# Optimization experiments

Measured on AMD Instinct MI355X. Metric: run time of the kernel, lower is better.

The kernel has to match this reference:

```python
import jax, jax.numpy as jnp
import numpy as np

N = 1024
C = 50000
D = 128
M_MARGIN = 0.35
S_SCALE = 30.0
LAMDA = 0.01


def setup_inputs() -> dict:
    key = jax.random.key(0)
    k1, k2, k3 = jax.random.split(key, 3)
    feature = jax.random.normal(k1, (N, D), dtype=jnp.float32)
    weight = jax.random.normal(k2, (C, D), dtype=jnp.float32)
    label = jax.random.randint(k3, (N,), 0, C, dtype=jnp.int64)
    return {"feature": feature, "weight": weight, "label": label}


def reference(feature, weight, label):
    eps = 1e-8  # torch CosineSimilarity eps
    f = feature / jnp.maximum(jnp.linalg.norm(feature, axis=-1, keepdims=True), eps)
    w = weight / jnp.maximum(jnp.linalg.norm(weight, axis=-1, keepdims=True), eps)
    cos = jnp.einsum("nd,cd->nc", f, w)  # [N, C] cosine similarities
    onehot = jax.nn.one_hot(label, C, dtype=cos.dtype)  # [N, C]
    # CosFace: subtract margin m from the target-class cosine, scale by s
    logits = S_SCALE * (cos - M_MARGIN * onehot)
    target_logit = S_SCALE * (jnp.take_along_axis(cos, label[:, None], axis=1)[:, 0] - M_MARGIN)
    # -log( exp(t) / (exp(t) + sum_{j != y} exp(s*cos_j)) ) = logsumexp(logits) - t
    lse = jax.nn.logsumexp(logits, axis=-1)  # [N]
    loss_lmc = jnp.mean(lse - target_logit)
    # center loss: 0.5 * sum_i ||f_i - w_{y_i}||^2
    diff = feature - weight[label]
    loss_c = 0.5 * jnp.sum(diff * diff)
    return loss_lmc + LAMDA * loss_c
```

## Files before the change

kernel.cpp:

```cpp
#include <hip/hip_runtime.h>

#define N_ROWS   1024
#define D_DIM    128
#define C_CLS    50000
#define C_PAD    50048
#define NCT64    782
#define NG       128
#define NPART    256
#define S_SCALE  30.0f
#define M_MARGIN 0.35f
#define EXP2_SCALE 43.2808512266689f
#define EXP2M      15.1482979293341f
#define LN2        0.6931471805599453f

typedef short s8v __attribute__((ext_vector_type(8)));
typedef float f4v __attribute__((ext_vector_type(4)));

__device__ inline unsigned short f2bf(float f) {
    unsigned u = __float_as_uint(f);
    u += 0x7FFF + ((u >> 16) & 1);
    return (unsigned short)(u >> 16);
}
__device__ inline float bf2f(unsigned short h) {
    return __uint_as_float(((unsigned)h) << 16);
}
__device__ inline void load_lds16(const char* src, unsigned char* lds) {
    __builtin_amdgcn_global_load_lds(
        (const __attribute__((address_space(1))) void*)src,
        (__attribute__((address_space(3))) void*)lds, 16, 0, 0);
}

__global__ void norm_rows_fused(const float* __restrict__ weight,
                                const float* __restrict__ feature,
                                unsigned short* __restrict__ what,
                                unsigned short* __restrict__ fhat) {
    int wid = threadIdx.x >> 6, lane = threadIdx.x & 63;
    int half = lane >> 5, l32 = lane & 31;
    int B = blockIdx.x;

    const float* src;
    unsigned short* dst;
    int rowBase, isW;
    float scale;
    if (B < 6272) {
        int x = B & 7, q = B >> 3;
        int ct = x + 8 * (q >> 3);
        if (ct >= NCT64) return;
        rowBase = ct * 64 + (q & 7) * 8;
        src = weight; dst = what; scale = 1.0f; isW = 1;
    } else {
        rowBase = (B - 6272) * 8;
        src = feature; dst = fhat; scale = EXP2_SCALE; isW = 0;
    }

    int srcRow = rowBase + wid * 2 + half;
    int valid = isW ? (srcRow < C_CLS) : 1;

    float4 v = make_float4(0.f, 0.f, 0.f, 0.f);
    if (valid) v = ((const float4*)src)[(size_t)srcRow * 32 + l32];
    float ss = v.x * v.x + v.y * v.y + v.z * v.z + v.w * v.w;
    #pragma unroll
    for (int s = 1; s < 32; s <<= 1) ss += __shfl_xor(ss, s, 32);
    float inv = valid ? scale / fmaxf(sqrtf(ss), 1e-8f) : 0.f;
    ushort4 o;
    o.x = f2bf(v.x * inv); o.y = f2bf(v.y * inv);
    o.z = f2bf(v.z * inv); o.w = f2bf(v.w * inv);
    ((ushort4*)dst)[(size_t)srcRow * 32 + l32] = o;
}

__global__ __launch_bounds__(256, 3)
void gemm_exp_kernel(const short* __restrict__ fhat,
                     const short* __restrict__ what,
                     float* __restrict__ part2) {
    __shared__ __align__(16) unsigned char smem[32768];
    const int g   = blockIdx.x;
    const int rt  = blockIdx.y;
    const int tid = threadIdx.x;
    const int wid = tid >> 6;
    const int lane = tid & 63;
    const int lrow = lane & 15;
    const int kgrp = lane >> 4;
    const int wrow = wid >> 1;
    const int wcol = wid & 1;
    const int nt = (g < 14) ? 7 : 6;
    const int rot = ((g >> 3) + rt) % nt;

    const char* aSrc  = (const char*)fhat + (size_t)rt * 32768;
    const char* bBase = (const char*)what;

    #pragma unroll
    for (int i = 0; i < 8; i++) {
        int o = wid * 8192 + i * 1024 + lane * 16;
        int s = o ^ (((o >> 8) & 7) << 4);
        load_lds16(aSrc + s, smem + o);
    }
    __syncthreads();

    s8v afr[4][4];
    #pragma unroll
    for (int kk = 0; kk < 4; kk++)
        #pragma unroll
        for (int m = 0; m < 4; m++) {
            int row = wrow * 64 + m * 16 + lrow;
            int b = (row * 256 + kk * 64 + kgrp * 16) ^ ((row & 7) << 4);
            afr[kk][m] = *(const s8v*)(smem + b);
        }
    __syncthreads();

    int vb[2][4];
    #pragma unroll
    for (int n = 0; n < 2; n++)
        #pragma unroll
        for (int kk = 0; kk < 4; kk++) {
            int row = wcol * 32 + n * 16 + lrow;
            vb[n][kk] = (row * 256 + kk * 64 + kgrp * 16) ^ ((row & 7) << 4);
        }

    {
        const char* src = bBase + (size_t)(g + 128 * rot) * 16384;
        #pragma unroll
        for (int i = 0; i < 4; i++) {
            int o = wid * 4096 + i * 1024 + lane * 16;
            int s = o ^ (((o >> 8) & 7) << 4);
            load_lds16(src + s, smem + o);
        }
    }

    float esum[4][4];
    #pragma unroll
    for (int m = 0; m < 4; m++)
        #pragma unroll
        for (int j = 0; j < 4; j++) esum[m][j] = 0.f;

    const f4v FZERO = {0.f, 0.f, 0.f, 0.f};

    for (int i = 0; i < nt; ++i) {
        int t = i + rot; if (t >= nt) t -= nt;
        const int ct = g + 128 * t;
        __syncthreads();

        if (i + 1 < nt) {
            int tn = t + 1; if (tn >= nt) tn -= nt;
            const char* src = bBase + (size_t)(g + 128 * tn) * 16384;
            unsigned char* dstb = smem + ((i + 1) & 1) * 16384;
            #pragma unroll
            for (int ii = 0; ii < 4; ii++) {
                int o = wid * 4096 + ii * 1024 + lane * 16;
                int s = o ^ (((o >> 8) & 7) << 4);
                load_lds16(src + s, dstb + o);
            }
        }

        const unsigned char* bb = smem + (i & 1) * 16384;
        f4v acc[4][2];

        {
            s8v b0 = *(const s8v*)(bb + vb[0][0]);
            s8v b1 = *(const s8v*)(bb + vb[1][0]);
            #pragma unroll
            for (int m = 0; m < 4; m++) {
                acc[m][0] = __builtin_amdgcn_mfma_f32_16x16x32_bf16(
                    afr[0][m], b0, FZERO, 0, 0, 0);
                acc[m][1] = __builtin_amdgcn_mfma_f32_16x16x32_bf16(
                    afr[0][m], b1, FZERO, 0, 0, 0);
            }
        }
        #pragma unroll
        for (int kk = 1; kk < 4; kk++) {
            s8v b0 = *(const s8v*)(bb + vb[0][kk]);
            s8v b1 = *(const s8v*)(bb + vb[1][kk]);
            #pragma unroll
            for (int m = 0; m < 4; m++) {
                acc[m][0] = __builtin_amdgcn_mfma_f32_16x16x32_bf16(
                    afr[kk][m], b0, acc[m][0], 0, 0, 0);
                acc[m][1] = __builtin_amdgcn_mfma_f32_16x16x32_bf16(
                    afr[kk][m], b1, acc[m][1], 0, 0, 0);
            }
        }

        if (ct != NCT64 - 1) {
            #pragma unroll
            for (int m = 0; m < 4; m++)
                #pragma unroll
                for (int n = 0; n < 2; n++)
                    #pragma unroll
                    for (int j = 0; j < 4; j++)
                        esum[m][j] += __builtin_amdgcn_exp2f(acc[m][n][j]);
        } else {
            #pragma unroll
            for (int n = 0; n < 2; n++) {
                int gc = ct * 64 + wcol * 32 + n * 16 + lrow;
                #pragma unroll
                for (int m = 0; m < 4; m++)
                    #pragma unroll
                    for (int j = 0; j < 4; j++)
                        if (gc < C_CLS)
                            esum[m][j] += __builtin_amdgcn_exp2f(acc[m][n][j]);
            }
        }
    }

    #pragma unroll
    for (int m = 0; m < 4; m++)
        #pragma unroll
        for (int j = 0; j < 4; j++) {
            float v = esum[m][j];
            v += __shfl_xor(v, 1, 64);
            v += __shfl_xor(v, 2, 64);
            v += __shfl_xor(v, 4, 64);
            v += __shfl_xor(v, 8, 64);
            if (lrow == 0) {
                int row = rt * 128 + wrow * 64 + m * 16 + kgrp * 4 + j;
                part2[(size_t)row * NPART + g * 2 + wcol] = v;
            }
        }
}

__global__ void finalize_rows_kernel(const float* __restrict__ part2,
                                     const unsigned short* __restrict__ fhat,
                                     const unsigned short* __restrict__ what,
                                     const float* __restrict__ feature,
                                     const float* __restrict__ weight,
                                     const int* __restrict__ label,
                                     float* __restrict__ rowval) {
    int wid = threadIdx.x >> 6, lane = threadIdx.x & 63;
    int n = blockIdx.x * 4 + wid;
    int y = label[n];

    const float* p = part2 + (size_t)n * NPART;
    float S = p[lane] + p[64 + lane] + p[128 + lane] + p[192 + lane];

    float2 f2 = ((const float2*)feature)[(size_t)n * 64 + lane];
    float2 w2 = ((const float2*)weight)[(size_t)y * 64 + lane];
    float dx = f2.x - w2.x, dy = f2.y - w2.y;
    float cl = dx * dx + dy * dy;

    ushort2 fh = ((const ushort2*)fhat)[(size_t)n * 64 + lane];
    ushort2 wh = ((const ushort2*)what)[(size_t)y * 64 + lane];
    float cys = bf2f(fh.x) * bf2f(wh.x) + bf2f(fh.y) * bf2f(wh.y);

    #pragma unroll
    for (int s = 1; s < 64; s <<= 1) {
        S   += __shfl_xor(S, s, 64);
        cl  += __shfl_xor(cl, s, 64);
        cys += __shfl_xor(cys, s, 64);
    }
    if (lane == 0) {
        float t2 = cys - EXP2M;
        float Sp = S - __builtin_amdgcn_exp2f(cys) + __builtin_amdgcn_exp2f(t2);
        rowval[n] = (logf(Sp) - LN2 * t2) * (1.0f / (float)N_ROWS) + 0.005f * cl;
    }
}

__global__ void reduce_final_kernel(const float* __restrict__ rowval, float* __restrict__ out) {
    __shared__ float sbuf[4];
    int t = threadIdx.x;
    float v = rowval[t] + rowval[t + 256] + rowval[t + 512] + rowval[t + 768];
    #pragma unroll
    for (int s = 1; s < 64; s <<= 1) v += __shfl_xor(v, s, 64);
    if ((t & 63) == 0) sbuf[t >> 6] = v;
    __syncthreads();
    if (t == 0) out[0] = sbuf[0] + sbuf[1] + sbuf[2] + sbuf[3];
}

extern "C" void kernel_launch(void* const* d_in, const int* in_sizes, int n_in,
                              void* d_out, int out_size, void* d_ws, size_t ws_size,
                              hipStream_t stream) {
    const float* feature = (const float*)d_in[0];
    const float* weight  = (const float*)d_in[1];
    const int*   label   = (const int*)d_in[2];

    const size_t WS_NEEDED = 14127104;
    if (ws_size < WS_NEEDED) return;

    char* ws = (char*)d_ws;
    unsigned short* what = (unsigned short*)ws;
    unsigned short* fhat = (unsigned short*)(ws + 12812288);
    float*         part2 = (float*)(ws + 13074432);
    float*        rowval = (float*)(ws + 14123008);

    norm_rows_fused<<<dim3(6400), 256, 0, stream>>>(weight, feature, what, fhat);
    gemm_exp_kernel<<<dim3(NG, 8), 256, 0, stream>>>((const short*)fhat, (const short*)what, part2);
    finalize_rows_kernel<<<dim3(N_ROWS / 4), 256, 0, stream>>>(part2, fhat, what, feature, weight,
                                                               label, rowval);
    reduce_final_kernel<<<1, 256, 0, stream>>>(rowval, (float*)d_out);
}
```

Before: 35.90 us.

## Software-pipeline MFMA tiles with exp accumulation and drop tile rotation

Restructures the class-tile loop so the MFMA for tile i+1 is issued before the exp2 accumulation of tile i, with the accumulators ping-ponged between two register sets. This is meant to overlap the transcendental VALU work with matrix-core work. It also removes the per-block rotation of the tile start, which spread concurrent blocks across different weight tiles, so all blocks now begin at the same tile. The extra accumulator set raises register pressure under the 3-blocks-per-CU launch bound. Masking is applied only to the last tile, which holds because that is the only tile that can be the padded one.

```diff
diff --git a/kernel.cpp b/kernel.cpp
--- a/kernel.cpp
+++ b/kernel.cpp
@@ -66,6 +66,64 @@
     o.x = f2bf(v.x * inv); o.y = f2bf(v.y * inv);
     o.z = f2bf(v.z * inv); o.w = f2bf(v.w * inv);
     ((ushort4*)dst)[(size_t)srcRow * 32 + l32] = o;
+}
+
+__device__ __forceinline__ void stage4(const char* src, unsigned char* dstb,
+                                       int wid, int lane) {
+    #pragma unroll
+    for (int ii = 0; ii < 4; ii++) {
+        int o = wid * 4096 + ii * 1024 + lane * 16;
+        int s = o ^ (((o >> 8) & 7) << 4);
+        load_lds16(src + s, dstb + o);
+    }
+}
+
+__device__ __forceinline__ void mfma_tile(const unsigned char* bb, const int (&vb)[2][4],
+                                          const s8v (&afr)[4][4], f4v (&acc)[4][2]) {
+    const f4v FZERO = {0.f, 0.f, 0.f, 0.f};
+    {
+        s8v b0 = *(const s8v*)(bb + vb[0][0]);
+        s8v b1 = *(const s8v*)(bb + vb[1][0]);
+        #pragma unroll
+        for (int m = 0; m < 4; m++) {
+            acc[m][0] = __builtin_amdgcn_mfma_f32_16x16x32_bf16(afr[0][m], b0, FZERO, 0, 0, 0);
+            acc[m][1] = __builtin_amdgcn_mfma_f32_16x16x32_bf16(afr[0][m], b1, FZERO, 0, 0, 0);
+        }
+    }
+    #pragma unroll
+    for (int kk = 1; kk < 4; kk++) {
+        s8v b0 = *(const s8v*)(bb + vb[0][kk]);
+        s8v b1 = *(const s8v*)(bb + vb[1][kk]);
+        #pragma unroll
+        for (int m = 0; m < 4; m++) {
+            acc[m][0] = __builtin_amdgcn_mfma_f32_16x16x32_bf16(afr[kk][m], b0, acc[m][0], 0, 0, 0);
+            acc[m][1] = __builtin_amdgcn_mfma_f32_16x16x32_bf16(afr[kk][m], b1, acc[m][1], 0, 0, 0);
+        }
+    }
+}
+
+__device__ __forceinline__ void exp_acc(const f4v (&acc)[4][2], float (&esum)[4][4]) {
+    #pragma unroll
+    for (int m = 0; m < 4; m++)
+        #pragma unroll
+        for (int n = 0; n < 2; n++)
+            #pragma unroll
+            for (int j = 0; j < 4; j++)
+                esum[m][j] += __builtin_amdgcn_exp2f(acc[m][n][j]);
+}
+
+__device__ __forceinline__ void exp_acc_masked(const f4v (&acc)[4][2], float (&esum)[4][4],
+                                               int ct, int wcol, int lrow) {
+    #pragma unroll
+    for (int n = 0; n < 2; n++) {
+        int gc = ct * 64 + wcol * 32 + n * 16 + lrow;
+        #pragma unroll
+        for (int m = 0; m < 4; m++)
+            #pragma unroll
+            for (int j = 0; j < 4; j++)
+                if (gc < C_CLS)
+                    esum[m][j] += __builtin_amdgcn_exp2f(acc[m][n][j]);
+    }
 }
 
 __global__ __launch_bounds__(256, 3)
@@ -83,7 +141,6 @@
     const int wrow = wid >> 1;
     const int wcol = wid & 1;
     const int nt = (g < 14) ? 7 : 6;
-    const int rot = ((g >> 3) + rt) % nt;
 
     const char* aSrc  = (const char*)fhat + (size_t)rt * 32768;
     const char* bBase = (const char*)what;
@@ -116,15 +173,7 @@
             vb[n][kk] = (row * 256 + kk * 64 + kgrp * 16) ^ ((row & 7) << 4);
         }
 
-    {
-        const char* src = bBase + (size_t)(g + 128 * rot) * 16384;
-        #pragma unroll
-        for (int i = 0; i < 4; i++) {
-            int o = wid * 4096 + i * 1024 + lane * 16;
-            int s = o ^ (((o >> 8) & 7) << 4);
-            load_lds16(src + s, smem + o);
-        }
-    }
+    stage4(bBase + (size_t)g * 16384, smem, wid, lane);
 
     float esum[4][4];
     #pragma unroll
@@ -132,72 +181,36 @@
         #pragma unroll
         for (int j = 0; j < 4; j++) esum[m][j] = 0.f;
 
-    const f4v FZERO = {0.f, 0.f, 0.f, 0.f};
-
-    for (int i = 0; i < nt; ++i) {
-        int t = i + rot; if (t >= nt) t -= nt;
-        const int ct = g + 128 * t;
+    f4v pA[4][2], pB[4][2];
+
+    __syncthreads();
+    if (nt > 1) stage4(bBase + (size_t)(g + 128) * 16384, smem + 16384, wid, lane);
+    mfma_tile(smem, vb, afr, pA);
+
+    int i = 1;
+    while (i < nt) {
         __syncthreads();
-
-        if (i + 1 < nt) {
-            int tn = t + 1; if (tn >= nt) tn -= nt;
-            const char* src = bBase + (size_t)(g + 128 * tn) * 16384;
-            unsigned char* dstb = smem + ((i + 1) & 1) * 16384;
-            #pragma unroll
-            for (int ii = 0; ii < 4; ii++) {
-                int o = wid * 4096 + ii * 1024 + lane * 16;
-                int s = o ^ (((o >> 8) & 7) << 4);
-                load_lds16(src + s, dstb + o);
-            }
-        }
-
-        const unsigned char* bb = smem + (i & 1) * 16384;
-        f4v acc[4][2];
-
-        {
-            s8v b0 = *(const s8v*)(bb + vb[0][0]);
-            s8v b1 = *(const s8v*)(bb + vb[1][0]);
-            #pragma unroll
-            for (int m = 0; m < 4; m++) {
-                acc[m][0] = __builtin_amdgcn_mfma_f32_16x16x32_bf16(
-                    afr[0][m], b0, FZERO, 0, 0, 0);
-                acc[m][1] = __builtin_amdgcn_mfma_f32_16x16x32_bf16(
-                    afr[0][m], b1, FZERO, 0, 0, 0);
-            }
-        }
-        #pragma unroll
-        for (int kk = 1; kk < 4; kk++) {
-            s8v b0 = *(const s8v*)(bb + vb[0][kk]);
-            s8v b1 = *(const s8v*)(bb + vb[1][kk]);
-            #pragma unroll
-            for (int m = 0; m < 4; m++) {
-                acc[m][0] = __builtin_amdgcn_mfma_f32_16x16x32_bf16(
-                    afr[kk][m], b0, acc[m][0], 0, 0, 0);
-                acc[m][1] = __builtin_amdgcn_mfma_f32_16x16x32_bf16(
-                    afr[kk][m], b1, acc[m][1], 0, 0, 0);
-            }
-        }
-
-        if (ct != NCT64 - 1) {
-            #pragma unroll
-            for (int m = 0; m < 4; m++)
-                #pragma unroll
-                for (int n = 0; n < 2; n++)
-                    #pragma unroll
-                    for (int j = 0; j < 4; j++)
-                        esum[m][j] += __builtin_amdgcn_exp2f(acc[m][n][j]);
-        } else {
-            #pragma unroll
-            for (int n = 0; n < 2; n++) {
-                int gc = ct * 64 + wcol * 32 + n * 16 + lrow;
-                #pragma unroll
-                for (int m = 0; m < 4; m++)
-                    #pragma unroll
-                    for (int j = 0; j < 4; j++)
-                        if (gc < C_CLS)
-                            esum[m][j] += __builtin_amdgcn_exp2f(acc[m][n][j]);
-            }
-        }
+        if (i + 1 < nt)
+            stage4(bBase + (size_t)(g + 128 * (i + 1)) * 16384, smem, wid, lane);
+        mfma_tile(smem + 16384, vb, afr, pB);
+        exp_acc(pA, esum);
+        ++i;
+        if (i >= nt) break;
+        __syncthreads();
+        if (i + 1 < nt)
+            stage4(bBase + (size_t)(g + 128 * (i + 1)) * 16384, smem + 16384, wid, lane);
+        mfma_tile(smem, vb, afr, pA);
+        exp_acc(pB, esum);
+        ++i;
+    }
+
+    const int ctLast = g + 128 * (nt - 1);
+    if (nt & 1) {
+        if (ctLast != NCT64 - 1) exp_acc(pA, esum);
+        else                     exp_acc_masked(pA, esum, ctLast, wcol, lrow);
+    } else {
+        if (ctLast != NCT64 - 1) exp_acc(pB, esum);
+        else                     exp_acc_masked(pB, esum, ctLast, wcol, lrow);
     }
 
     #pragma unroll
```

Result: slower. 45.17 us (+25.8%).
